# Optimization experiments

Measured on AMD Instinct MI355X. Metric: run time of the kernel, lower is better.

The kernel has to match this reference:

```python
import jax, jax.numpy as jnp
import numpy as np

BATCH, IN, HID, OMID, OUT = 8192, 64, 1024, 128, 1
MAX_ITER = 8
EPS = 1e-3


def setup_inputs() -> dict:
    key = jax.random.key(0)
    ks = jax.random.split(key, 32)
    s_in, s_h = 1.0 / np.sqrt(IN), 1.0 / np.sqrt(HID)
    d = {"x": jax.random.normal(ks[0], (BATCH, IN), jnp.float32)}
    names = ["i", "f", "c", "o"]
    for j, n in enumerate(names):
        d[f"Wx{n}"] = jax.random.uniform(ks[1 + 4 * j], (HID, IN), jnp.float32, -s_in, s_in)
        d[f"bx{n}"] = jax.random.uniform(ks[2 + 4 * j], (HID,), jnp.float32, -s_in, s_in)
        d[f"Wh{n}"] = jax.random.uniform(ks[3 + 4 * j], (HID, HID), jnp.float32, -s_h, s_h)
        d[f"bh{n}"] = jax.random.uniform(ks[4 + 4 * j], (HID,), jnp.float32, -s_h, s_h)
    d["W_halt"] = jax.random.uniform(ks[20], (1, HID), jnp.float32, -s_h, s_h)
    d["b_halt"] = jax.random.uniform(ks[21], (1,), jnp.float32, -s_h, s_h)
    d["W1"] = jax.random.uniform(ks[22], (OMID, HID), jnp.float32, -s_h, s_h)
    d["b1"] = jax.random.uniform(ks[23], (OMID,), jnp.float32, -s_h, s_h)
    s_m = 1.0 / np.sqrt(OMID)
    d["W2"] = jax.random.uniform(ks[24], (OUT, OMID), jnp.float32, -s_m, s_m)
    d["b2"] = jax.random.uniform(ks[25], (OUT,), jnp.float32, -s_m, s_m)
    return d


def _act_forward(x, Wxi, bxi, Whi, bhi, Wxf, bxf, Whf, bhf, Wxc, bxc, Whc, bhc,
                 Wxo, bxo, Who, bho, W_halt, b_halt, W1, b1, W2, b2):
    B = x.shape[0]
    state0 = jnp.zeros((B, HID), x.dtype)
    cell0 = jnp.zeros((B, HID), x.dtype)
    p0 = jnp.zeros((B,), x.dtype)
    active0 = jnp.ones((B,), bool)

    def step(carry, t):
        state, cell, p_sum, active = carry
        # four LSTM-style gates (computed dense; masked update == torch's gather/scatter)
        i_g = jax.nn.sigmoid(x @ Wxi.T + bxi + state @ Whi.T + bhi)
        f_g = jax.nn.sigmoid(x @ Wxf.T + bxf + state @ Whf.T + bhf)
        c_g = jnp.tanh(x @ Wxc.T + bxc + state @ Whc.T + bhc)
        o_g = jax.nn.sigmoid(x @ Wxo.T + bxo + state @ Who.T + bho)
        am = active[:, None]
        cell = jnp.where(am, f_g * cell + i_g * c_g, cell)
        state = jnp.where(am, o_g * jnp.tanh(cell), state)
        out = jax.nn.sigmoid(jax.nn.relu(state @ W1.T + b1) @ W2.T + b2)  # (B, OUT)
        h = jax.nn.sigmoid(state @ W_halt.T + b_halt)[:, 0]               # (B,)
        p_new = p_sum + h
        last = t == MAX_ITER - 1
        finished = active & ((p_new >= 1.0 - EPS) | last)
        halt_rec = jnp.where(finished, 1.0 - p_sum, jnp.where(active, h, 0.0))
        p_sum = jnp.where(finished, 1.0, jnp.where(active, p_new, p_sum))
        out_rec = jnp.where(am, out, 0.0)
        active = active & ~finished
        return (state, cell, p_sum, active), (out_rec, halt_rec)

    _, (outs, halts) = jax.lax.scan(step, (state0, cell0, p0, active0), jnp.arange(MAX_ITER))
    # outs: (T, B, OUT), halts: (T, B); final = sum_t out_t * p_halt_t
    return jnp.einsum("tbo,tb->bo", outs, halts)


def reference(x, Wxi, bxi, Whi, bhi, Wxf, bxf, Whf, bhf, Wxc, bxc, Whc, bhc,
              Wxo, bxo, Who, bho, W_halt, b_halt, W1, b1, W2, b2):
    return _act_forward(x, Wxi, bxi, Whi, bhi, Wxf, bxf, Whf, bhf, Wxc, bxc, Whc, bhc,
                        Wxo, bxo, Who, bho, W_halt, b_halt, W1, b1, W2, b2)
```

## Files before the change

### kernel.cpp

```cpp
#include <hip/hip_runtime.h>
#include <hip/hip_bf16.h>

#define BATCH 8192
#define IN_DIM 64
#define HID 1024
#define KTOT 1088
#define NGATES 4096
#define OMID 128
#define NP 256
#define MAX_ITER 8

#define TM 128
#define TN 128
#define TK 64
#define GTM 256
#define GTN 256
#define TAILB 64

typedef __attribute__((ext_vector_type(8))) short short8;
typedef __attribute__((ext_vector_type(4))) float float4v;

__device__ __forceinline__ float bf2f(short s) {
    union { float f; unsigned u; } v; v.u = ((unsigned)(unsigned short)s) << 16; return v.f;
}
__device__ __forceinline__ short f2bf(float f) {
    union { float f; unsigned u; } v; v.f = f;
    unsigned r = v.u + 0x7fff + ((v.u >> 16) & 1);
    return (short)(r >> 16);
}
__device__ __forceinline__ float sigmoidf_(float x) {
    float xc = fminf(fmaxf(x, -30.f), 30.f);
    return 1.f / (1.f + __expf(-xc));
}
__device__ __forceinline__ float tanhf_(float x) {
    float xc = fminf(fmaxf(x, -15.f), 15.f);
    float e = __expf(2.f * xc);
    return (e - 1.f) / (e + 1.f);
}
__device__ __forceinline__ int aload(const int* p) {
    return __hip_atomic_load((int*)p, __ATOMIC_RELAXED, __HIP_MEMORY_SCOPE_AGENT);
}
__device__ __forceinline__ void astore(int* p, int v) {
    __hip_atomic_store(p, v, __ATOMIC_RELAXED, __HIP_MEMORY_SCOPE_AGENT);
}

__device__ __forceinline__ void gbar(int* bar, int phase, int tid) {
    __syncthreads();
    if (tid == 0) {
        __threadfence();
        __hip_atomic_fetch_add(bar, 1, __ATOMIC_ACQ_REL, __HIP_MEMORY_SCOPE_AGENT);
        while (aload(bar) < TAILB * phase)
            __builtin_amdgcn_s_sleep(8);
        __threadfence();
    }
    __syncthreads();
}

__device__ __forceinline__ void gates_epilogue(
    const float4v (&acc)[4][4], int m0, int bx, int wave, int lane, int first,
    const float* __restrict__ bias_g, float* __restrict__ cell,
    short* __restrict__ Sout, const int* __restrict__ ridx, int n_act)
{
    const int wm = wave & 1, wn = wave >> 1;
    const int colq = lane & 15, q = lane >> 4;
    const int G = bx * 2 + wn;
    const int h = G * 16 + colq;
    const float bi  = bias_g[G * 64 +  0 + colq];
    const float bff = bias_g[G * 64 + 16 + colq];
    const float bc  = bias_g[G * 64 + 32 + colq];
    const float bo  = bias_g[G * 64 + 48 + colq];
#pragma unroll
    for (int i = 0; i < 4; ++i) {
        const int pbase = m0 + wm * 64 + i * 16 + q * 4;
#pragma unroll
        for (int r = 0; r < 4; ++r) {
            const int pos = pbase + r;
            if (pos < n_act) {
                const int row = ridx[pos];
                const float ig = sigmoidf_(acc[i][0][r] + bi);
                const float fg = sigmoidf_(acc[i][1][r] + bff);
                const float cg = tanhf_(acc[i][2][r] + bc);
                const float og = sigmoidf_(acc[i][3][r] + bo);
                const size_t ci = (size_t)row * HID + h;
                const float c = first ? (ig * cg) : (fg * cell[ci] + ig * cg);
                cell[ci] = c;
                Sout[(size_t)row * HID + h] = f2bf(og * tanhf_(c));
            }
        }
    }
}

__global__ __launch_bounds__(512, 1) void gates_k(
    const short* __restrict__ S, const short* __restrict__ XB,
    const short* __restrict__ B,
    const float* __restrict__ bias_g, int nK, int hidK, int first,
    float* __restrict__ cell, short* __restrict__ Sout,
    const int* __restrict__ ridx, const int* __restrict__ cnt, int t)
{
    __shared__ short As[2][GTM * TK];
    __shared__ short Bs[2][GTN * TK];
    const int n_act = cnt[t];
    const int tid  = threadIdx.x;
    const int wave = tid >> 6, lane = tid & 63;
    const int wm2 = wave >> 2, wn4 = wave & 3;
    const int colq = lane & 15, q = lane >> 4;
    const int lrow8 = lane >> 3;
    const int lk    = (((lane & 7) ^ lrow8) * 8);
    const int n0 = blockIdx.x * GTN;
    const int xq = colq & 7;
    const int abase = (wm2 * 128 + colq) * TK;
    const int bbase = (wn4 * 64  + colq) * TK;

    for (int by = blockIdx.y; by * GTM < n_act; by += gridDim.y) {
        const int m0 = by * GTM;

        int rows_[4];
        const short* gb[4];
#pragma unroll
        for (int it = 0; it < 4; ++it) {
            const int rr = wave * 32 + it * 8 + lrow8;
            rows_[it] = ridx[m0 + rr];
            gb[it] = B + (size_t)(n0 + rr) * KTOT + lk;
        }

        float4v acc[8][4];
#pragma unroll
        for (int i = 0; i < 8; ++i)
#pragma unroll
            for (int j = 0; j < 4; ++j) acc[i][j] = (float4v)0.f;

        auto stage = [&](int ki, int buf) {
            const int kk = ki * TK;
            const bool fromS = (kk < hidK);
#pragma unroll
            for (int it = 0; it < 4; ++it) {
                const int dst = (wave * 32 + it * 8) * TK;
                const short* sa = fromS
                    ? (S  + (size_t)rows_[it] * HID    + kk + lk)
                    : (XB + (size_t)rows_[it] * IN_DIM + lk);
                __builtin_amdgcn_global_load_lds(
                    (const __attribute__((address_space(1))) void*)sa,
                    (__attribute__((address_space(3))) void*)(As[buf] + dst), 16, 0, 0);
                __builtin_amdgcn_global_load_lds(
                    (const __attribute__((address_space(1))) void*)(gb[it] + kk),
                    (__attribute__((address_space(3))) void*)(Bs[buf] + dst), 16, 0, 0);
            }
        };

        stage(0, 0);
        __syncthreads();

        for (int ki = 0; ki < nK; ++ki) {
            const int cur = ki & 1;
            if (ki + 1 < nK) stage(ki + 1, cur ^ 1);
            const short* Ac = As[cur];
            const short* Bc = Bs[cur];
#pragma unroll
            for (int c2 = 0; c2 < 2; ++c2) {
                const int xt = ((q + 4 * c2) ^ xq) << 3;
                short8 af[8], bf[4];
#pragma unroll
                for (int i = 0; i < 8; ++i)
                    af[i] = *(const short8*)(Ac + abase + i * (16 * TK) + xt);
#pragma unroll
                for (int j = 0; j < 4; ++j)
                    bf[j] = *(const short8*)(Bc + bbase + j * (16 * TK) + xt);
#pragma unroll
                for (int i = 0; i < 8; ++i)
#pragma unroll
                    for (int j = 0; j < 4; ++j)
                        acc[i][j] = __builtin_amdgcn_mfma_f32_16x16x32_bf16(af[i], bf[j], acc[i][j], 0, 0, 0);
            }
            __syncthreads();
        }

        const int G = blockIdx.x * 4 + wn4;
        const int h = G * 16 + colq;
        const float bi  = bias_g[G * 64 +  0 + colq];
        const float bff = bias_g[G * 64 + 16 + colq];
        const float bc  = bias_g[G * 64 + 32 + colq];
        const float bo  = bias_g[G * 64 + 48 + colq];
#pragma unroll
        for (int i = 0; i < 8; ++i) {
            const int pbase = m0 + wm2 * 128 + i * 16 + q * 4;
#pragma unroll
            for (int r = 0; r < 4; ++r) {
                const int pos = pbase + r;
                if (pos < n_act) {
                    const int row = ridx[pos];
                    const float ig = sigmoidf_(acc[i][0][r] + bi);
                    const float fg = sigmoidf_(acc[i][1][r] + bff);
                    const float cg = tanhf_(acc[i][2][r] + bc);
                    const float og = sigmoidf_(acc[i][3][r] + bo);
                    const size_t ci = (size_t)row * HID + h;
                    const float c = first ? (ig * cg) : (fg * cell[ci] + ig * cg);
                    cell[ci] = c;
                    Sout[(size_t)row * HID + h] = f2bf(og * tanhf_(c));
                }
            }
        }
    }
}

__device__ __forceinline__ void gates_tile(
    short* As, short* Bs, int tid,
    const short* __restrict__ S, const short* __restrict__ XB,
    const short* __restrict__ B,
    const float* __restrict__ bias_g,
    float* __restrict__ cell, short* __restrict__ Sout,
    const int* __restrict__ ridx, int n_act, int m0, int bx)
{
    const int wave = tid >> 6, lane = tid & 63;
    const int wm = wave & 1, wn = wave >> 1;
    const int colq = lane & 15, q = lane >> 4;
    const int lrow8 = lane >> 3;
    const int lk    = (((lane & 7) ^ lrow8) * 8);
    const int n0 = bx * TN;

    int aoff[4][2], boff[4][2];
#pragma unroll
    for (int i = 0; i < 4; ++i) {
        const int Ra = wm * 64 + i * 16 + colq;
        const int Rb = wn * 64 + i * 16 + colq;
#pragma unroll
        for (int c2 = 0; c2 < 2; ++c2) {
            const int C = q + 4 * c2;
            aoff[i][c2] = Ra * TK + ((C ^ (Ra & 7)) << 3);
            boff[i][c2] = Rb * TK + ((C ^ (Rb & 7)) << 3);
        }
    }

    float4v acc[4][4];
#pragma unroll
    for (int i = 0; i < 4; ++i)
#pragma unroll
        for (int j = 0; j < 4; ++j) acc[i][j] = (float4v)0.f;

    const short* gaS[4];
    const short* gaX[4];
    const short* gb[4];
#pragma unroll
    for (int it = 0; it < 4; ++it) {
        const int rr = (wave * 4 + it) * 8;
        const int r0 = ridx[m0 + rr + lrow8];
        gaS[it] = S + (size_t)r0 * HID + lk;
        gaX[it] = XB + (size_t)r0 * IN_DIM + lk;
        gb[it]  = B + (size_t)(n0 + rr + lrow8) * KTOT + lk;
    }

    for (int ki = 0; ki < KTOT / TK; ++ki) {
        const bool fromS = (ki * TK < HID);
#pragma unroll
        for (int it = 0; it < 4; ++it) {
            const int rr = (wave * 4 + it) * 8;
            const short* a0 = fromS ? gaS[it] : gaX[it];
            __builtin_amdgcn_global_load_lds(
                (const __attribute__((address_space(1))) void*)a0,
                (__attribute__((address_space(3))) void*)(As + rr * TK), 16, 0, 0);
            __builtin_amdgcn_global_load_lds(
                (const __attribute__((address_space(1))) void*)gb[it],
                (__attribute__((address_space(3))) void*)(Bs + rr * TK), 16, 0, 0);
            gaS[it] += TK; gb[it] += TK;
        }
        __syncthreads();
#pragma unroll
        for (int c2 = 0; c2 < 2; ++c2) {
            short8 af[4], bf[4];
#pragma unroll
            for (int i = 0; i < 4; ++i) {
                af[i] = *(const short8*)(As + aoff[i][c2]);
                bf[i] = *(const short8*)(Bs + boff[i][c2]);
            }
#pragma unroll
            for (int i = 0; i < 4; ++i)
#pragma unroll
                for (int j = 0; j < 4; ++j)
                    acc[i][j] = __builtin_amdgcn_mfma_f32_16x16x32_bf16(af[i], bf[j], acc[i][j], 0, 0, 0);
        }
        __syncthreads();
    }

    gates_epilogue(acc, m0, bx, wave, lane, 0, bias_g, cell, Sout, ridx, n_act);
    __syncthreads();
}

__device__ __forceinline__ void midfin_tile(
    short* As, short* Bs, int tid,
    const short* __restrict__ Snew, const short* __restrict__ P,
    const float* __restrict__ bias_p, const float* __restrict__ W_halt,
    const float* __restrict__ W2, const float* __restrict__ b2,
    float* __restrict__ outp, float* __restrict__ p_sum,
    const int* __restrict__ rprev, int* __restrict__ rnext,
    int* __restrict__ cnt, int t, int m0, int n_act)
{
    const int wave = tid >> 6, lane = tid & 63;
    const int wm = wave & 1, wn = wave >> 1;
    const int colq = lane & 15, q = lane >> 4;
    const int lrow8 = lane >> 3;
    const int lk    = (((lane & 7) ^ lrow8) * 8);

    float4v acc[4][4];
#pragma unroll
    for (int i = 0; i < 4; ++i)
#pragma unroll
        for (int j = 0; j < 4; ++j) acc[i][j] = (float4v)0.f;

    const short* ga[4];
    const short* gb[4];
#pragma unroll
    for (int it = 0; it < 4; ++it) {
        const int rr = (wave * 4 + it) * 8;
        ga[it] = Snew + (size_t)rprev[m0 + rr + lrow8] * HID + lk;
        gb[it] = P + (size_t)(rr + lrow8) * HID + lk;
    }
    int aoff[4][2], boff[4][2];
#pragma unroll
    for (int i = 0; i < 4; ++i) {
        const int Ra = wm * 64 + i * 16 + colq;
        const int Rb = wn * 64 + i * 16 + colq;
#pragma unroll
        for (int c2 = 0; c2 < 2; ++c2) {
            const int C = q + 4 * c2;
            aoff[i][c2] = Ra * TK + ((C ^ (Ra & 7)) << 3);
            boff[i][c2] = Rb * TK + ((C ^ (Rb & 7)) << 3);
        }
    }

    for (int k0 = 0; k0 < HID; k0 += TK) {
#pragma unroll
        for (int it = 0; it < 4; ++it) {
            const int rr = (wave * 4 + it) * 8;
            __builtin_amdgcn_global_load_lds(
                (const __attribute__((address_space(1))) void*)ga[it],
                (__attribute__((address_space(3))) void*)(As + rr * TK), 16, 0, 0);
            __builtin_amdgcn_global_load_lds(
                (const __attribute__((address_space(1))) void*)gb[it],
                (__attribute__((address_space(3))) void*)(Bs + rr * TK), 16, 0, 0);
            ga[it] += TK; gb[it] += TK;
        }
        __syncthreads();
#pragma unroll
        for (int c2 = 0; c2 < 2; ++c2) {
            short8 af[4], bf[4];
#pragma unroll
            for (int i = 0; i < 4; ++i) {
                af[i] = *(const short8*)(As + aoff[i][c2]);
                bf[i] = *(const short8*)(Bs + boff[i][c2]);
            }
#pragma unroll
            for (int i = 0; i < 4; ++i)
#pragma unroll
                for (int j = 0; j < 4; ++j)
                    acc[i][j] = __builtin_amdgcn_mfma_f32_16x16x32_bf16(af[i], bf[j], acc[i][j], 0, 0, 0);
        }
        __syncthreads();
    }

    float* red  = (float*)As;
    float* hbuf = ((float*)As) + 256;

    for (int s = 0; s < 32; ++s) {
        const int lr = wave * 32 + s;
        const int row = rprev[m0 + lr];
        const short* Ar = Snew + (size_t)row * HID + lane * 16;
        const short8 v0 = *(const short8*)Ar;
        const short8 v1 = *(const short8*)(Ar + 8);
        const float* Wh = W_halt + lane * 16;
        float hv = 0.f;
#pragma unroll
        for (int e = 0; e < 8; ++e) hv += bf2f(v0[e]) * Wh[e];
#pragma unroll
        for (int e = 0; e < 8; ++e) hv += bf2f(v1[e]) * Wh[8 + e];
#pragma unroll
        for (int o = 32; o > 0; o >>= 1) hv += __shfl_down(hv, o);
        if (lane == 0) hbuf[lr] = hv;
    }

    float pr[4][4];
#pragma unroll
    for (int i = 0; i < 4; ++i)
#pragma unroll
        for (int r = 0; r < 4; ++r) pr[i][r] = 0.f;
#pragma unroll
    for (int j = 0; j < 4; ++j) {
        const int col = wn * 64 + j * 16 + colq;
        const float b = bias_p[col];
        const float w2 = W2[col];
#pragma unroll
        for (int i = 0; i < 4; ++i)
#pragma unroll
            for (int r = 0; r < 4; ++r)
                pr[i][r] += fmaxf(acc[i][j][r] + b, 0.f) * w2;
    }
#pragma unroll
    for (int i = 0; i < 4; ++i)
#pragma unroll
        for (int r = 0; r < 4; ++r) {
            float v = pr[i][r];
            v += __shfl_down(v, 8, 16);
            v += __shfl_down(v, 4, 16);
            v += __shfl_down(v, 2, 16);
            v += __shfl_down(v, 1, 16);
            if (colq == 0)
                red[((((wn * 2) + wm) * 4 + i) * 4 + q) * 4 + r] = v;
        }
    __syncthreads();

    if (tid < TM) {
        const int pos = m0 + tid;
        if (pos < n_act) {
            const int lwm = tid >> 6, i = (tid >> 4) & 3, lq = (tid >> 2) & 3, r = tid & 3;
            const float odot = red[((lwm * 4 + i) * 4 + lq) * 4 + r]
                             + red[(((2 + lwm) * 4 + i) * 4 + lq) * 4 + r];
            const int row = rprev[pos];
            const float ov = sigmoidf_(odot + b2[0]);
            const float h  = sigmoidf_(hbuf[tid] + bias_p[OMID]);
            const float ps = p_sum[row];
            const float pn = ps + h;
            const bool fin = (pn >= 1.f - 1e-3f) || (t == MAX_ITER - 1);
            const float halt = fin ? (1.f - ps) : h;
            outp[row] += ov * halt;
            p_sum[row] = fin ? 1.f : pn;
            if (!fin) {
                const int d = atomicAdd(&cnt[t + 1], 1);
                astore(&rnext[d], row);
            }
        }
    }
    __syncthreads();
}

__global__ __launch_bounds__(256) void midfin_k(
    const short* __restrict__ Snew, const short* __restrict__ P,
    const float* __restrict__ bias_p, const float* __restrict__ W_halt,
    const float* __restrict__ W2, const float* __restrict__ b2,
    float* __restrict__ outp, float* __restrict__ p_sum,
    const int* __restrict__ rprev, int* __restrict__ rnext,
    int* __restrict__ cnt, int t)
{
    __shared__ short As[TM * TK];
    __shared__ short Bs[TN * TK];
    const int n_act = cnt[t];
    for (int tile = blockIdx.x; tile * TM < n_act; tile += gridDim.x)
        midfin_tile(As, Bs, threadIdx.x, Snew, P, bias_p, W_halt, W2, b2,
                    outp, p_sum, rprev, rnext, cnt, t, tile * TM, n_act);
}

__global__ __launch_bounds__(256) void tail_k(
    const short* __restrict__ Wg, const float* __restrict__ bias_g,
    const short* __restrict__ P, const float* __restrict__ bias_p,
    const float* __restrict__ W_halt, const float* __restrict__ W2,
    const float* __restrict__ b2,
    short* __restrict__ S0, short* __restrict__ S1,
    const short* __restrict__ XB,
    float* __restrict__ cell, float* __restrict__ outp,
    float* __restrict__ p_sum,
    int* __restrict__ ridx0, int* __restrict__ ridx1,
    int* __restrict__ cnt, int* __restrict__ bar)
{
    __shared__ short As[TM * TK];
    __shared__ short Bs[TN * TK];
    const int tid = threadIdx.x;
    int phase = 0;
    int t = 2;
    while (true) {
        short* Snew = (t & 1) ? S0 : S1;
        const int* rprev = (t & 1) ? ridx1 : ridx0;
        int* rnext = (t & 1) ? ridx0 : ridx1;
        const int n = aload(&cnt[t]);
        for (int tile = blockIdx.x; tile * TM < n; tile += gridDim.x)
            midfin_tile(As, Bs, tid, Snew, P, bias_p, W_halt, W2, b2,
                        outp, p_sum, rprev, rnext, cnt, t, tile * TM, n);
        if (t == MAX_ITER - 1) break;
        ++phase; gbar(bar, phase, tid);
        const int n1 = aload(&cnt[t + 1]);
        if (n1 == 0) break;
        {
            short* Sot = (t & 1) ? S1 : S0;
            const int ntiles = ((n1 + TM - 1) / TM) * (NGATES / TN);
            for (int e = blockIdx.x; e < ntiles; e += gridDim.x)
                gates_tile(As, Bs, tid, Snew, XB, Wg, bias_g, cell, Sot,
                           rnext, n1, (e >> 5) * TM, e & 31);
        }
        ++phase; gbar(bar, phase, tid);
        ++t;
    }
}

#define SETUP_XB    (BATCH * IN_DIM)
#define SETUP_WG    (NGATES * KTOT)
#define SETUP_P     (NP * HID)
#define SETUP_TOT   (SETUP_XB + SETUP_WG + SETUP_P)
__global__ __launch_bounds__(256) void setup_k(
    const float* __restrict__ x,
    const float* __restrict__ Whi, const float* __restrict__ Whf,
    const float* __restrict__ Whc, const float* __restrict__ Who,
    const float* __restrict__ Wxi, const float* __restrict__ Wxf,
    const float* __restrict__ Wxc, const float* __restrict__ Wxo,
    const float* __restrict__ bxi, const float* __restrict__ bhi,
    const float* __restrict__ bxf, const float* __restrict__ bhf,
    const float* __restrict__ bxc, const float* __restrict__ bhc,
    const float* __restrict__ bxo, const float* __restrict__ bho,
    const float* __restrict__ W1, const float* __restrict__ b1,
    const float* __restrict__ W_halt, const float* __restrict__ b_halt,
    short* __restrict__ XB,
    float* __restrict__ p_sum,
    int* __restrict__ ridx0, int* __restrict__ ridx1, int* __restrict__ cnt,
    int* __restrict__ bar, float* __restrict__ outp,
    short* __restrict__ Wg, float* __restrict__ bias_g,
    short* __restrict__ P, float* __restrict__ bias_p)
{
    int idx = blockIdx.x * 256 + threadIdx.x;
    if (idx < SETUP_XB) {
        const int row = idx >> 6, k = idx & 63;
        XB[idx] = f2bf(x[idx]);
        if (k == 0) {
            p_sum[row] = 0.f;
            outp[row] = 0.f;
            ridx0[row] = row;
            ridx1[row] = 0;
        }
        if (row == 0 && k <= MAX_ITER) cnt[k] = (k == 0) ? BATCH : 0;
        if (row == 1 && k == 0) bar[0] = 0;
        return;
    }
    idx -= SETUP_XB;
    if (idx < SETUP_WG) {
        const int n = idx / KTOT, k = idx - n * KTOT;
        const int G = n >> 6, g = (n >> 4) & 3, q = n & 15;
        const int h = G * 16 + q;
        const float* Wh = (g == 0) ? Whi : (g == 1) ? Whf : (g == 2) ? Whc : Who;
        const float* Wx = (g == 0) ? Wxi : (g == 1) ? Wxf : (g == 2) ? Wxc : Wxo;
        const float v = (k < HID) ? Wh[h * HID + k] : Wx[h * IN_DIM + (k - HID)];
        Wg[idx] = f2bf(v);
        if (k == 0) {
            const float* bx = (g == 0) ? bxi : (g == 1) ? bxf : (g == 2) ? bxc : bxo;
            const float* bh = (g == 0) ? bhi : (g == 1) ? bhf : (g == 2) ? bhc : bho;
            bias_g[n] = bx[h] + bh[h];
        }
        return;
    }
    idx -= SETUP_WG;
    if (idx < SETUP_P) {
        const int n = idx >> 10, k = idx & 1023;
        const float v = (n < OMID) ? W1[n * HID + k] : (n == OMID ? W_halt[k] : 0.f);
        P[idx] = f2bf(v);
        if (k == 0) bias_p[n] = (n < OMID) ? b1[n] : (n == OMID ? b_halt[0] : 0.f);
    }
}

extern "C" void kernel_launch(void* const* d_in, const int* in_sizes, int n_in,
                              void* d_out, int out_size, void* d_ws, size_t ws_size,
                              hipStream_t stream) {
    const float* x    = (const float*)d_in[0];
    const float* Wxi  = (const float*)d_in[1];
    const float* bxi  = (const float*)d_in[2];
    const float* Whi  = (const float*)d_in[3];
    const float* bhi  = (const float*)d_in[4];
    const float* Wxf  = (const float*)d_in[5];
    const float* bxf  = (const float*)d_in[6];
    const float* Whf  = (const float*)d_in[7];
    const float* bhf  = (const float*)d_in[8];
    const float* Wxc  = (const float*)d_in[9];
    const float* bxc  = (const float*)d_in[10];
    const float* Whc  = (const float*)d_in[11];
    const float* bhc  = (const float*)d_in[12];
    const float* Wxo  = (const float*)d_in[13];
    const float* bxo  = (const float*)d_in[14];
    const float* Who  = (const float*)d_in[15];
    const float* bho  = (const float*)d_in[16];
    const float* W_halt = (const float*)d_in[17];
    const float* b_halt = (const float*)d_in[18];
    const float* W1   = (const float*)d_in[19];
    const float* b1   = (const float*)d_in[20];
    const float* W2   = (const float*)d_in[21];
    const float* b2   = (const float*)d_in[22];

    char* p = (char*)d_ws;
    auto carve = [&](size_t bytes) { char* r = p; p += (bytes + 255) & ~(size_t)255; return r; };
    short* S0     = (short*)carve((size_t)BATCH * HID * 2);
    short* S1     = (short*)carve((size_t)BATCH * HID * 2);
    short* XB     = (short*)carve((size_t)BATCH * IN_DIM * 2);
    short* Wg     = (short*)carve((size_t)NGATES * KTOT * 2);
    float* bias_g = (float*)carve((size_t)NGATES * 4);
    short* P      = (short*)carve((size_t)NP * HID * 2);
    float* bias_p = (float*)carve((size_t)NP * 4);
    float* cell   = (float*)carve((size_t)BATCH * HID * 4);
    float* p_sum  = (float*)carve((size_t)BATCH * 4);
    int*   ridx0  = (int*)carve((size_t)BATCH * 4);
    int*   ridx1  = (int*)carve((size_t)BATCH * 4);
    int*   cnt    = (int*)carve((size_t)(MAX_ITER + 1) * 4);
    int*   bar    = (int*)carve(256);
    float* outp   = (float*)d_out;

    setup_k<<<(SETUP_TOT + 255) / 256, 256, 0, stream>>>(
        x, Whi, Whf, Whc, Who, Wxi, Wxf, Wxc, Wxo,
        bxi, bhi, bxf, bhf, bxc, bhc, bxo, bho,
        W1, b1, W_halt, b_halt,
        XB, p_sum, ridx0, ridx1, cnt, bar, outp,
        Wg, bias_g, P, bias_p);

    gates_k<<<dim3(NGATES / GTN, 16), 512, 0, stream>>>(
        S0, XB, Wg + HID, bias_g, 1, 0, 1, cell, S1, ridx0, cnt, 0);
    midfin_k<<<64, 256, 0, stream>>>(
        S1, P, bias_p, W_halt, W2, b2, outp, p_sum, ridx0, ridx1, cnt, 0);
    gates_k<<<dim3(NGATES / GTN, 16), 512, 0, stream>>>(
        S1, XB, Wg, bias_g, KTOT / TK, HID, 0, cell, S0, ridx1, cnt, 1);
    midfin_k<<<64, 256, 0, stream>>>(
        S0, P, bias_p, W_halt, W2, b2, outp, p_sum, ridx1, ridx0, cnt, 1);
    gates_k<<<dim3(NGATES / GTN, 16), 512, 0, stream>>>(
        S0, XB, Wg, bias_g, KTOT / TK, HID, 0, cell, S1, ridx0, cnt, 2);
    tail_k<<<TAILB, 256, 0, stream>>>(
        Wg, bias_g, P, bias_p, W_halt, W2, b2,
        S0, S1, XB, cell, outp, p_sum, ridx0, ridx1, cnt, bar);
}
```

Measured before the change: 471.5 us.

## Prefetch two K-tiles ahead with explicit waitcnt and barriers in gate GEMM

Restructures the double-buffered gate GEMM main loop so that two stages are issued up front. Each iteration loads all LDS fragments into registers, barriers, and then immediately refills the just-freed buffer with tile ki+2 before running the MFMAs. Partial vmcnt waits replace the full __syncthreads, so global-to-LDS loads overlap with compute more deeply. In exchange it uses more registers for the fragments and hand-written waitcnt counts that must match the number of loads issued per stage.

```diff
diff --git a/kernel.cpp b/kernel.cpp
--- a/kernel.cpp
+++ b/kernel.cpp
@@ -148,30 +148,50 @@
         };
 
         stage(0, 0);
-        __syncthreads();
+        if (nK > 1) {
+            stage(1, 1);
+            asm volatile("s_waitcnt vmcnt(8)" ::: "memory");
+        } else {
+            asm volatile("s_waitcnt vmcnt(0)" ::: "memory");
+        }
+        asm volatile("s_barrier" ::: "memory");
 
         for (int ki = 0; ki < nK; ++ki) {
             const int cur = ki & 1;
-            if (ki + 1 < nK) stage(ki + 1, cur ^ 1);
             const short* Ac = As[cur];
             const short* Bc = Bs[cur];
+
+            short8 af[2][8], bf[2][4];
 #pragma unroll
             for (int c2 = 0; c2 < 2; ++c2) {
                 const int xt = ((q + 4 * c2) ^ xq) << 3;
-                short8 af[8], bf[4];
 #pragma unroll
                 for (int i = 0; i < 8; ++i)
-                    af[i] = *(const short8*)(Ac + abase + i * (16 * TK) + xt);
+                    af[c2][i] = *(const short8*)(Ac + abase + i * (16 * TK) + xt);
 #pragma unroll
                 for (int j = 0; j < 4; ++j)
-                    bf[j] = *(const short8*)(Bc + bbase + j * (16 * TK) + xt);
+                    bf[c2][j] = *(const short8*)(Bc + bbase + j * (16 * TK) + xt);
+            }
+
+            if (ki + 2 < nK) {
+                asm volatile("s_waitcnt lgkmcnt(0)" ::: "memory");
+                asm volatile("s_barrier" ::: "memory");
+                stage(ki + 2, cur);
+            }
+
+#pragma unroll
+            for (int c2 = 0; c2 < 2; ++c2)
 #pragma unroll
                 for (int i = 0; i < 8; ++i)
 #pragma unroll
                     for (int j = 0; j < 4; ++j)
-                        acc[i][j] = __builtin_amdgcn_mfma_f32_16x16x32_bf16(af[i], bf[j], acc[i][j], 0, 0, 0);
-            }
-            __syncthreads();
+                        acc[i][j] = __builtin_amdgcn_mfma_f32_16x16x32_bf16(af[c2][i], bf[c2][j], acc[i][j], 0, 0, 0);
+
+            if (ki + 2 < nK)
+                asm volatile("s_waitcnt vmcnt(8) lgkmcnt(0)" ::: "memory");
+            else
+                asm volatile("s_waitcnt vmcnt(0) lgkmcnt(0)" ::: "memory");
+            asm volatile("s_barrier" ::: "memory");
         }
 
         const int G = blockIdx.x * 4 + wn4;
```

Measured after the change: 523.0 us. +10.9%, slower.

## Remap gates blocks across XCDs and shrink midfin tiles to 32 rows

Applied to the files above, without the earlier changes.

The gates kernel now remaps its linear block index so that blocks sharing the same weight column tiles and row tiles land on the same XCD, which should improve L2 reuse on the multi-die chip. The midfin output-head tile drops from 128 to 32 batch rows, with each wave owning 32 of the 128 hidden columns. Grid size rises from 64 to 256 blocks so more CUs take part in this low-occupancy stage. The trade-off is that the P weights are reloaded more often per row and each block does less MFMA work relative to its loads and syncs. The tail kernel keeps only 64 blocks, so it loops over more, smaller tiles.

```diff
diff --git a/kernel.cpp b/kernel.cpp
--- a/kernel.cpp
+++ b/kernel.cpp
@@ -13,6 +13,7 @@
 #define TM 128
 #define TN 128
 #define TK 64
+#define TMF 32
 #define GTM 256
 #define GTN 256
 #define TAILB 64
@@ -106,12 +107,21 @@
     const int colq = lane & 15, q = lane >> 4;
     const int lrow8 = lane >> 3;
     const int lk    = (((lane & 7) ^ lrow8) * 8);
-    const int n0 = blockIdx.x * GTN;
     const int xq = colq & 7;
     const int abase = (wm2 * 128 + colq) * TK;
     const int bbase = (wn4 * 64  + colq) * TK;
 
-    for (int by = blockIdx.y; by * GTM < n_act; by += gridDim.y) {
+    int bx, byS;
+    {
+        const int lin  = (int)blockIdx.x + 16 * (int)blockIdx.y;
+        const int xcd  = lin & 7;
+        const int slot = lin >> 3;
+        bx  = (xcd & 1) * 8 + (slot & 7);
+        byS = (xcd >> 1) * 4 + (slot >> 3);
+    }
+    const int n0 = bx * GTN;
+
+    for (int by = byS; by * GTM < n_act; by += 16) {
         const int m0 = by * GTM;
 
         int rows_[4];
@@ -174,7 +184,7 @@
             __syncthreads();
         }
 
-        const int G = blockIdx.x * 4 + wn4;
+        const int G = bx * 4 + wn4;
         const int h = G * 16 + colq;
         const float bi  = bias_g[G * 64 +  0 + colq];
         const float bff = bias_g[G * 64 + 16 + colq];
@@ -294,73 +304,58 @@
     int* __restrict__ cnt, int t, int m0, int n_act)
 {
     const int wave = tid >> 6, lane = tid & 63;
-    const int wm = wave & 1, wn = wave >> 1;
     const int colq = lane & 15, q = lane >> 4;
     const int lrow8 = lane >> 3;
     const int lk    = (((lane & 7) ^ lrow8) * 8);
-
-    float4v acc[4][4];
-#pragma unroll
-    for (int i = 0; i < 4; ++i)
-#pragma unroll
-        for (int j = 0; j < 4; ++j) acc[i][j] = (float4v)0.f;
-
-    const short* ga[4];
-    const short* gb[4];
-#pragma unroll
-    for (int it = 0; it < 4; ++it) {
-        const int rr = (wave * 4 + it) * 8;
-        ga[it] = Snew + (size_t)rprev[m0 + rr + lrow8] * HID + lk;
-        gb[it] = P + (size_t)(rr + lrow8) * HID + lk;
-    }
-    int aoff[4][2], boff[4][2];
-#pragma unroll
-    for (int i = 0; i < 4; ++i) {
-        const int Ra = wm * 64 + i * 16 + colq;
-        const int Rb = wn * 64 + i * 16 + colq;
+    const int xq = colq & 7;
+
+    float4v acc[2][2];
+#pragma unroll
+    for (int mi = 0; mi < 2; ++mi)
+#pragma unroll
+        for (int nj = 0; nj < 2; ++nj) acc[mi][nj] = (float4v)0.f;
+
+    const short* ga = Snew + (size_t)rprev[m0 + wave * 8 + lrow8] * HID + lk;
+    const short* gbp[4];
+#pragma unroll
+    for (int g = 0; g < 4; ++g)
+        gbp[g] = P + (size_t)(wave * 32 + g * 8 + lrow8) * HID + lk;
+
+    for (int k0 = 0; k0 < HID; k0 += TK) {
+        __builtin_amdgcn_global_load_lds(
+            (const __attribute__((address_space(1))) void*)(ga + k0),
+            (__attribute__((address_space(3))) void*)(As + (wave * 8) * TK), 16, 0, 0);
+#pragma unroll
+        for (int g = 0; g < 4; ++g)
+            __builtin_amdgcn_global_load_lds(
+                (const __attribute__((address_space(1))) void*)(gbp[g] + k0),
+                (__attribute__((address_space(3))) void*)(Bs + (wave * 32 + g * 8) * TK), 16, 0, 0);
+        __syncthreads();
 #pragma unroll
         for (int c2 = 0; c2 < 2; ++c2) {
-            const int C = q + 4 * c2;
-            aoff[i][c2] = Ra * TK + ((C ^ (Ra & 7)) << 3);
-            boff[i][c2] = Rb * TK + ((C ^ (Rb & 7)) << 3);
-        }
-    }
-
-    for (int k0 = 0; k0 < HID; k0 += TK) {
-#pragma unroll
-        for (int it = 0; it < 4; ++it) {
-            const int rr = (wave * 4 + it) * 8;
-            __builtin_amdgcn_global_load_lds(
-                (const __attribute__((address_space(1))) void*)ga[it],
-                (__attribute__((address_space(3))) void*)(As + rr * TK), 16, 0, 0);
-            __builtin_amdgcn_global_load_lds(
-                (const __attribute__((address_space(1))) void*)gb[it],
-                (__attribute__((address_space(3))) void*)(Bs + rr * TK), 16, 0, 0);
-            ga[it] += TK; gb[it] += TK;
+            const int xt = ((q + 4 * c2) ^ xq) << 3;
+            short8 af[2], bf[2];
+#pragma unroll
+            for (int mi = 0; mi < 2; ++mi)
+                af[mi] = *(const short8*)(As + (mi * 16 + colq) * TK + xt);
+#pragma unroll
+            for (int nj = 0; nj < 2; ++nj)
+                bf[nj] = *(const short8*)(Bs + (wave * 32 + nj * 16 + colq) * TK + xt);
+#pragma unroll
+            for (int mi = 0; mi < 2; ++mi)
+#pragma unroll
+                for (int nj = 0; nj < 2; ++nj)
+                    acc[mi][nj] = __builtin_amdgcn_mfma_f32_16x16x32_bf16(af[mi], bf[nj], acc[mi][nj], 0, 0, 0);
         }
         __syncthreads();
-#pragma unroll
-        for (int c2 = 0; c2 < 2; ++c2) {
-            short8 af[4], bf[4];
-#pragma unroll
-            for (int i = 0; i < 4; ++i) {
-                af[i] = *(const short8*)(As + aoff[i][c2]);
-                bf[i] = *(const short8*)(Bs + boff[i][c2]);
-            }
-#pragma unroll
-            for (int i = 0; i < 4; ++i)
-#pragma unroll
-                for (int j = 0; j < 4; ++j)
-                    acc[i][j] = __builtin_amdgcn_mfma_f32_16x16x32_bf16(af[i], bf[j], acc[i][j], 0, 0, 0);
-        }
-        __syncthreads();
     }
 
     float* red  = (float*)As;
-    float* hbuf = ((float*)As) + 256;
-
-    for (int s = 0; s < 32; ++s) {
-        const int lr = wave * 32 + s;
+    float* hbuf = ((float*)As) + 128;
+
+#pragma unroll
+    for (int s = 0; s < 8; ++s) {
+        const int lr = wave * 8 + s;
         const int row = rprev[m0 + lr];
         const short* Ar = Snew + (size_t)row * HID + lane * 16;
         const short8 v0 = *(const short8*)Ar;
@@ -376,42 +371,44 @@
         if (lane == 0) hbuf[lr] = hv;
     }
 
-    float pr[4][4];
-#pragma unroll
-    for (int i = 0; i < 4; ++i)
-#pragma unroll
-        for (int r = 0; r < 4; ++r) pr[i][r] = 0.f;
-#pragma unroll
-    for (int j = 0; j < 4; ++j) {
-        const int col = wn * 64 + j * 16 + colq;
+    float pr[2][4];
+#pragma unroll
+    for (int mi = 0; mi < 2; ++mi)
+#pragma unroll
+        for (int r = 0; r < 4; ++r) pr[mi][r] = 0.f;
+#pragma unroll
+    for (int nj = 0; nj < 2; ++nj) {
+        const int col = wave * 32 + nj * 16 + colq;
         const float b = bias_p[col];
         const float w2 = W2[col];
 #pragma unroll
-        for (int i = 0; i < 4; ++i)
+        for (int mi = 0; mi < 2; ++mi)
 #pragma unroll
             for (int r = 0; r < 4; ++r)
-                pr[i][r] += fmaxf(acc[i][j][r] + b, 0.f) * w2;
-    }
-#pragma unroll
-    for (int i = 0; i < 4; ++i)
+                pr[mi][r] += fmaxf(acc[mi][nj][r] + b, 0.f) * w2;
+    }
+#pragma unroll
+    for (int mi = 0; mi < 2; ++mi)
 #pragma unroll
         for (int r = 0; r < 4; ++r) {
-            float v = pr[i][r];
+            float v = pr[mi][r];
             v += __shfl_down(v, 8, 16);
             v += __shfl_down(v, 4, 16);
             v += __shfl_down(v, 2, 16);
             v += __shfl_down(v, 1, 16);
             if (colq == 0)
-                red[((((wn * 2) + wm) * 4 + i) * 4 + q) * 4 + r] = v;
+                red[((wave * 2 + mi) * 4 + q) * 4 + r] = v;
         }
     __syncthreads();
 
-    if (tid < TM) {
+    if (tid < TMF) {
         const int pos = m0 + tid;
         if (pos < n_act) {
-            const int lwm = tid >> 6, i = (tid >> 4) & 3, lq = (tid >> 2) & 3, r = tid & 3;
-            const float odot = red[((lwm * 4 + i) * 4 + lq) * 4 + r]
-                             + red[(((2 + lwm) * 4 + i) * 4 + lq) * 4 + r];
+            const int mi = tid >> 4, lq = (tid >> 2) & 3, r = tid & 3;
+            float odot = 0.f;
+#pragma unroll
+            for (int w = 0; w < 4; ++w)
+                odot += red[((w * 2 + mi) * 4 + lq) * 4 + r];
             const int row = rprev[pos];
             const float ov = sigmoidf_(odot + b2[0]);
             const float h  = sigmoidf_(hbuf[tid] + bias_p[OMID]);
@@ -441,9 +438,9 @@
     __shared__ short As[TM * TK];
     __shared__ short Bs[TN * TK];
     const int n_act = cnt[t];
-    for (int tile = blockIdx.x; tile * TM < n_act; tile += gridDim.x)
+    for (int tile = blockIdx.x; tile * TMF < n_act; tile += gridDim.x)
         midfin_tile(As, Bs, threadIdx.x, Snew, P, bias_p, W_halt, W2, b2,
-                    outp, p_sum, rprev, rnext, cnt, t, tile * TM, n_act);
+                    outp, p_sum, rprev, rnext, cnt, t, tile * TMF, n_act);
 }
 
 __global__ __launch_bounds__(256) void tail_k(
@@ -468,9 +465,9 @@
         const int* rprev = (t & 1) ? ridx1 : ridx0;
         int* rnext = (t & 1) ? ridx0 : ridx1;
         const int n = aload(&cnt[t]);
-        for (int tile = blockIdx.x; tile * TM < n; tile += gridDim.x)
+        for (int tile = blockIdx.x; tile * TMF < n; tile += gridDim.x)
             midfin_tile(As, Bs, tid, Snew, P, bias_p, W_halt, W2, b2,
-                        outp, p_sum, rprev, rnext, cnt, t, tile * TM, n);
+                        outp, p_sum, rprev, rnext, cnt, t, tile * TMF, n);
         if (t == MAX_ITER - 1) break;
         ++phase; gbar(bar, phase, tid);
         const int n1 = aload(&cnt[t + 1]);
@@ -600,15 +597,15 @@
         XB, p_sum, ridx0, ridx1, cnt, bar, outp,
         Wg, bias_g, P, bias_p);
 
-    gates_k<<<dim3(NGATES / GTN, 16), 512, 0, stream>>>(
+    gates_k<<<dim3(16, 16), 512, 0, stream>>>(
         S0, XB, Wg + HID, bias_g, 1, 0, 1, cell, S1, ridx0, cnt, 0);
-    midfin_k<<<64, 256, 0, stream>>>(
+    midfin_k<<<256, 256, 0, stream>>>(
         S1, P, bias_p, W_halt, W2, b2, outp, p_sum, ridx0, ridx1, cnt, 0);
-    gates_k<<<dim3(NGATES / GTN, 16), 512, 0, stream>>>(
+    gates_k<<<dim3(16, 16), 512, 0, stream>>>(
         S1, XB, Wg, bias_g, KTOT / TK, HID, 0, cell, S0, ridx1, cnt, 1);
-    midfin_k<<<64, 256, 0, stream>>>(
+    midfin_k<<<256, 256, 0, stream>>>(
         S0, P, bias_p, W_halt, W2, b2, outp, p_sum, ridx1, ridx0, cnt, 1);
-    gates_k<<<dim3(NGATES / GTN, 16), 512, 0, stream>>>(
+    gates_k<<<dim3(16, 16), 512, 0, stream>>>(
         S0, XB, Wg, bias_g, KTOT / TK, HID, 0, cell, S1, ridx0, cnt, 2);
     tail_k<<<TAILB, 256, 0, stream>>>(
         Wg, bias_g, P, bias_p, W_halt, W2, b2,
```

After: 445.9 us. 1.06x faster.
